# Kernel tuning notes

Hardware: AMD Instinct MI355X
Metric: run time of the kernel (lower is better)

## Reference

```python
import jax, jax.numpy as jnp
import numpy as np

B, H, W = 1, 1024, 2048
NX = 2048
H_STEP = 6.0 / NX            # h = length_x / nx
COF = 1.0                    # TEMPER_COEFFICIENT
DIFF = 0.0                   # self.diff_coeff
WC0V = 651.83 * 202.412 * 0.001 / 2.0   # wc0 = WC0*TH0*0.001/THcell
C1, C2, C4, N_EXP, CT = 0.65248278, 0.002, 400.0, 0.5, 1.0
FLUX0 = 300.0                # self.flux value used inside evp()

# 3x3 'valid' stencils on the reflect-padded field (match torch conv2d cross-correlation)
def _dx(x):
    return 0.5 * (x[..., 1:-1, 2:] - x[..., 1:-1, :-2])

def _dy(x):
    return 0.5 * (x[..., 2:, 1:-1] - x[..., :-2, 1:-1])

def _lap(x):
    return (x[..., 1:-1, 2:] + x[..., 1:-1, :-2] + x[..., 2:, 1:-1]
            + x[..., :-2, 1:-1] - 4.0 * x[..., 1:-1, 1:-1])

def _evp(tmp, wc_bc):
    t = tmp + 273.15
    cp_a = (28.11 + 1.967e-3 * t + 4.802e-6 * t**2 - 1.966e-9 * t**3) / 28.97 * 1000.0
    cp_v = (32.24 + 1.923e-3 * t + 10.55e-6 * t**2 - 3.595e-9 * t**3) / 18.015 * 1000.0
    P_v = jnp.exp(23.2 - 3816.4 / (t - 46.1))
    x_v = 0.62198 * P_v / (101325.0 - P_v)
    x_a = 0.00725
    C3 = jnp.power(jnp.mean(wc_bc) / WC0V, N_EXP)
    porous = C1 * C2 * C3 * C4 * CT
    m_dot = FLUX0 / (cp_a + cp_v * x_a) * (x_v - x_a) * porous
    return m_dot


def _forward(layout, heat_ini, wc, heat, flow):
    u = flow[..., 0, :, :]                      # [B,H,W]
    v = flow[..., 1, :, :]
    b = layout[:, 1].squeeze()                  # [H,W] int boundary codes
    geom = layout[:, 0].astype(heat.dtype)      # [B,H,W]
    geom = geom.at[..., 0, :].set(1.0).at[..., -1, :].set(1.0)
    # in-place boundary edits, same order as torch
    b = (b.at[1, 1:].set(0).at[-2, 1:].set(0).at[:, 1].set(0)
          .at[:, -1].set(3).at[0, :].set(3).at[-1, :].set(3))

    wc_mask = (b > 3).astype(wc.dtype)          # [H,W], broadcasts like torch [1,1,H,W]
    wc_bc = wc * wc_mask
    bc_mask = (b != 1).astype(heat.dtype)       # set_bc(1, tmp=0): mask 0, value 0
    heat_bc = heat * bc_mask

    xp = jnp.pad(heat_bc, ((0, 0), (0, 0), (1, 1), (1, 1)), mode='reflect')
    m_dot = _evp(heat_bc, wc_bc)                # evp called twice with identical state
    src = 300.0 * H_STEP                        # self.src (evp_src returns 0)
    flux = 300.0 * H_STEP                       # self.flux at apply_Energy time

    dx_, dy_ = _dx(xp), _dy(xp)                 # [B,1,H,W]
    ad = heat_ini - 0.001 * (u * dx_ + v * dy_ - DIFF * _lap(xp) / H_STEP)
    wcv = WC0V - 0.001 * m_dot                  # self.wc(wc)

    extras = {0: 0.0, 2: 0.0, 3: 0.0,
              4: flux * dx_ + wcv, 5: -flux * dy_ + wcv,
              6: -flux * dx_ + wcv, 7: flux * dy_ + wcv,
              8: flux * (-dx_ + dy_) + wcv, 9: flux * (dy_ + dx_) + wcv,
              10: flux * (dx_ - dy_) + wcv, 11: flux * (-dx_ - dy_) + wcv}
    loss_eq = jnp.zeros_like(heat)
    eq_mask = jnp.zeros_like(b)
    for eq in [0, 2, 3, 4, 5, 6, 7, 8, 9, 10, 11]:   # fixed small set, not a data dim
        m = (b == eq)
        eq_mask = jnp.where(m, eq, eq_mask)
        loss_eq = loss_eq + m.astype(heat.dtype) * (ad + extras[eq])

    f = COF * jnp.abs(geom - 1.0) * src * H_STEP     # [B,H,W]
    energy_loss = jnp.mean((loss_eq - f[:, None]) ** 2)
    wc_loss = jnp.mean((WC0V * wc_mask - m_dot - wc_bc) ** 2)
    return energy_loss + wc_loss, heat_bc, eq_mask


def setup_inputs() -> dict:
    key = jax.random.key(0)
    k1, k2, k3, k4, k5 = jax.random.split(key, 5)
    layout = jax.random.randint(k1, (B, 2, H, W), 0, 12, dtype=jnp.int32)
    heat_ini = jax.random.normal(k2, (B, 1, H, W), dtype=jnp.float32)
    wc = jax.random.uniform(k3, (B, 1, H, W), dtype=jnp.float32)
    heat = jax.random.normal(k4, (B, 1, H, W), dtype=jnp.float32)
    flow = jax.random.normal(k5, (B, 2, H, W), dtype=jnp.float32)
    return {"layout": layout, "heat_ini": heat_ini, "wc": wc, "heat": heat, "flow": flow}


def reference(layout, heat_ini, wc, heat, flow):
    return _forward(layout, heat_ini, wc, heat, flow)
```

## Files before the change

kernel.cpp:

```cpp
#include <hip/hip_runtime.h>
#include <math.h>

#define H_ 1024
#define W_ 2048
#define HW_ (H_ * W_)
#define NB_ 2048

#define FLUXF     0.87890625f
#define F_FACT    0.002574920654296875f
#define WC0VF     65.96910698f
#define POROUS_K  0.521986224f

__device__ __forceinline__ int fix_b(int raw, int i, int j) {
    if (i == 0 || i == H_ - 1) return 3;
    if (j == W_ - 1) return 3;
    if (j == 1) return 0;
    if ((i == 1 || i == H_ - 2) && j >= 1) return 0;
    return raw;
}

__global__ __launch_bounds__(256)
void k_main(const int* __restrict__ layout, const float* __restrict__ heat_ini,
            const float* __restrict__ wc, const float* __restrict__ heat,
            const float* __restrict__ flow, float* __restrict__ out_hb,
            float* __restrict__ out_eq, float* __restrict__ ws) {
    int gid  = blockIdx.x * 256 + threadIdx.x;
    int idx4 = gid << 2;
    int i  = idx4 >> 11;
    int jb = idx4 & (W_ - 1);
    int im = (i == 0) ? 1 : i - 1;
    int ip = (i == H_ - 1) ? H_ - 2 : i + 1;
    const int* L1 = layout + HW_;

    int4   bc4 = *(const int4*)(L1 + idx4);
    int4   bu4 = *(const int4*)(L1 + im * W_ + jb);
    int4   bd4 = *(const int4*)(L1 + ip * W_ + jb);
    int4   g4  = *(const int4*)(layout + idx4);
    float4 hc4 = *(const float4*)(heat + idx4);
    float4 hu4 = *(const float4*)(heat + im * W_ + jb);
    float4 hd4 = *(const float4*)(heat + ip * W_ + jb);
    float4 hi4 = *(const float4*)(heat_ini + idx4);
    float4 w4  = *(const float4*)(wc + idx4);
    float4 u4  = *(const float4*)(flow + idx4);
    float4 v4  = *(const float4*)(flow + HW_ + idx4);

    float hl = 0.0f, hr = 0.0f; int bl = 0, br = 0;
    if (jb != 0)      { hl = heat[idx4 - 1]; bl = L1[idx4 - 1]; }
    if (jb != W_ - 4) { hr = heat[idx4 + 4]; br = L1[idx4 + 4]; }

    int   bcs[4] = {bc4.x, bc4.y, bc4.z, bc4.w};
    int   bus[4] = {bu4.x, bu4.y, bu4.z, bu4.w};
    int   bds[4] = {bd4.x, bd4.y, bd4.z, bd4.w};
    int   gs[4]  = {g4.x, g4.y, g4.z, g4.w};
    float hcs[4] = {hc4.x, hc4.y, hc4.z, hc4.w};
    float hus[4] = {hu4.x, hu4.y, hu4.z, hu4.w};
    float hds[4] = {hd4.x, hd4.y, hd4.z, hd4.w};
    float his[4] = {hi4.x, hi4.y, hi4.z, hi4.w};
    float wss[4] = {w4.x, w4.y, w4.z, w4.w};
    float us[4]  = {u4.x, u4.y, u4.z, u4.w};
    float vs[4]  = {v4.x, v4.y, v4.z, v4.w};

    int bfix[4];
    float hb6[6];
    hb6[0] = (fix_b(bl, i, jb - 1) != 1) ? hl : 0.0f;
    hb6[5] = (fix_b(br, i, jb + 4) != 1) ? hr : 0.0f;
    float4 ohb, oeq;
    float* pohb = &ohb.x; float* poeq = &oeq.x;
    #pragma unroll
    for (int k = 0; k < 4; k++) {
        int b = fix_b(bcs[k], i, jb + k);
        bfix[k] = b;
        float hbv = (b != 1) ? hcs[k] : 0.0f;
        hb6[k + 1] = hbv;
        pohb[k] = hbv;
        poeq[k] = (b == 1) ? 0.0f : (float)b;
    }
    *(float4*)(out_hb + idx4) = ohb;
    *(float4*)(out_eq + idx4) = oeq;

    float acc[7] = {0.f, 0.f, 0.f, 0.f, 0.f, 0.f, 0.f};
    #pragma unroll
    for (int k = 0; k < 4; k++) {
        int j = jb + k;
        int b = bfix[k];
        float dx = 0.5f * (hb6[k + 2] - hb6[k]);
        if (j == 0 || j == W_ - 1) dx = 0.0f;
        float hbu = (fix_b(bus[k], im, j) != 1) ? hus[k] : 0.0f;
        float hbd = (fix_b(bds[k], ip, j) != 1) ? hds[k] : 0.0f;
        float dy = 0.5f * (hbd - hbu);

        float ad = his[k] - 0.001f * (us[k] * dx + vs[k] * dy);

        float t  = hb6[k + 1] + 273.15f;
        float t2 = t * t, t3 = t2 * t;
        float cp_a = (28.11f + 0.001967f * t + 4.802e-6f * t2 - 1.966e-9f * t3)
                     * (1000.0f / 28.97f);
        float cp_v = (32.24f + 0.001923f * t + 1.055e-5f * t2 - 3.595e-9f * t3)
                     * (1000.0f / 18.015f);
        float P_v = expf(23.2f - 3816.4f / (t - 46.1f));
        float x_v = 0.62198f * P_v / (101325.0f - P_v);
        float q = 300.0f / (cp_a + cp_v * 0.00725f) * (x_v - 0.00725f);

        float f = (i == 0 || i == H_ - 1) ? 0.0f
                  : fabsf((float)gs[k] - 1.0f) * F_FACT;

        float a_e, c_e;
        if (b == 1) {
            a_e = -f; c_e = 0.0f;
        } else {
            float cx = (b == 4 || b == 9 || b == 10) ? 1.0f
                     : ((b == 6 || b == 8 || b == 11) ? -1.0f : 0.0f);
            float cy = (b == 7 || b == 8 || b == 9) ? 1.0f
                     : ((b == 5 || b == 10 || b == 11) ? -1.0f : 0.0f);
            float extra0 = (b >= 4) ? (FLUXF * (cx * dx + cy * dy) + WC0VF) : 0.0f;
            a_e = ad + extra0 - f;
            c_e = (b >= 4) ? (-0.001f * q) : 0.0f;
        }
        acc[1] += a_e * a_e;
        acc[2] += a_e * c_e;
        acc[3] += c_e * c_e;

        float wm  = (b > 3) ? 1.0f : 0.0f;
        float wcb = wm * wss[k];
        float aw  = WC0VF * wm - wcb;
        acc[0] += wcb;
        acc[4] += aw * aw;
        acc[5] += aw * q;
        acc[6] += q * q;
    }

    #pragma unroll
    for (int off = 32; off > 0; off >>= 1) {
        #pragma unroll
        for (int s = 0; s < 7; s++) acc[s] += __shfl_down(acc[s], off, 64);
    }
    __shared__ float red[4][7];
    int lane = threadIdx.x & 63, wid = threadIdx.x >> 6;
    if (lane == 0) {
        #pragma unroll
        for (int s = 0; s < 7; s++) red[wid][s] = acc[s];
    }
    __syncthreads();
    if (threadIdx.x == 0) {
        #pragma unroll
        for (int s = 0; s < 7; s++)
            ws[s * NB_ + blockIdx.x] =
                red[0][s] + red[1][s] + red[2][s] + red[3][s];
    }
}

__global__ __launch_bounds__(256)
void k_final(const float* __restrict__ ws, float* __restrict__ out) {
    __shared__ float sred[7][4];
    int tid = threadIdx.x;
    #pragma unroll
    for (int s = 0; s < 7; s++) {
        float a = 0.0f;
        for (int t = tid; t < NB_; t += 256) a += ws[s * NB_ + t];
        #pragma unroll
        for (int off = 32; off > 0; off >>= 1) a += __shfl_down(a, off, 64);
        if ((tid & 63) == 0) sred[s][tid >> 6] = a;
    }
    __syncthreads();
    if (tid == 0) {
        float S[7];
        #pragma unroll
        for (int s = 0; s < 7; s++)
            S[s] = sred[s][0] + sred[s][1] + sred[s][2] + sred[s][3];
        float mean_wc = S[0] * (1.0f / (float)HW_);
        float p = POROUS_K * sqrtf(mean_wc / WC0VF);
        float energy = S[1] + 2.0f * p * S[2] + p * p * S[3];
        float wcl    = S[4] - 2.0f * p * S[5] + p * p * S[6];
        out[0] = (energy + wcl) * (1.0f / (float)HW_);
    }
}

extern "C" void kernel_launch(void* const* d_in, const int* in_sizes, int n_in,
                              void* d_out, int out_size, void* d_ws, size_t ws_size,
                              hipStream_t stream) {
    const int*   layout   = (const int*)d_in[0];
    const float* heat_ini = (const float*)d_in[1];
    const float* wc       = (const float*)d_in[2];
    const float* heat     = (const float*)d_in[3];
    const float* flow     = (const float*)d_in[4];
    float* out = (float*)d_out;
    float* ws  = (float*)d_ws;

    float* out_hb = out + 1;
    float* out_eq = out + 1 + HW_;

    k_main<<<NB_, 256, 0, stream>>>(layout, heat_ini, wc, heat, flow,
                                    out_hb, out_eq, ws);
    k_final<<<1, 256, 0, stream>>>(ws, out);
}
```

Measured before the change: 127.1 us.

## Map one block per row with 8 elements per thread and LDS halo exchange

Each block now covers one full image row and each thread handles 8 contiguous elements, using two float4 loads per array. The masked heat row is staged in shared memory so the left and right neighbours for the x-derivative come from LDS rather than scalar global loads. The block count is halved, and the final reduction reads one float4 per thread. This adds a __syncthreads and raises register pressure from the doubled per-thread state.

```diff
diff --git a/kernel.cpp b/kernel.cpp
--- a/kernel.cpp
+++ b/kernel.cpp
@@ -4,7 +4,7 @@
 #define H_ 1024
 #define W_ 2048
 #define HW_ (H_ * W_)
-#define NB_ 2048
+#define NB_ 1024
 
 #define FLUXF     0.87890625f
 #define F_FACT    0.002574920654296875f
@@ -24,74 +24,72 @@
             const float* __restrict__ wc, const float* __restrict__ heat,
             const float* __restrict__ flow, float* __restrict__ out_hb,
             float* __restrict__ out_eq, float* __restrict__ ws) {
-    int gid  = blockIdx.x * 256 + threadIdx.x;
-    int idx4 = gid << 2;
-    int i  = idx4 >> 11;
-    int jb = idx4 & (W_ - 1);
-    int im = (i == 0) ? 1 : i - 1;
-    int ip = (i == H_ - 1) ? H_ - 2 : i + 1;
+    const int i  = blockIdx.x;
+    const int jb = threadIdx.x << 3;
+    const int im = (i == 0) ? 1 : i - 1;
+    const int ip = (i == H_ - 1) ? H_ - 2 : i + 1;
     const int* L1 = layout + HW_;
+    const int base  = i * W_ + jb;
+    const int baseu = im * W_ + jb;
+    const int based = ip * W_ + jb;
 
-    int4   bc4 = *(const int4*)(L1 + idx4);
-    int4   bu4 = *(const int4*)(L1 + im * W_ + jb);
-    int4   bd4 = *(const int4*)(L1 + ip * W_ + jb);
-    int4   g4  = *(const int4*)(layout + idx4);
-    float4 hc4 = *(const float4*)(heat + idx4);
-    float4 hu4 = *(const float4*)(heat + im * W_ + jb);
-    float4 hd4 = *(const float4*)(heat + ip * W_ + jb);
-    float4 hi4 = *(const float4*)(heat_ini + idx4);
-    float4 w4  = *(const float4*)(wc + idx4);
-    float4 u4  = *(const float4*)(flow + idx4);
-    float4 v4  = *(const float4*)(flow + HW_ + idx4);
+    int4   bc0 = *(const int4*)(L1 + base),      bc1 = *(const int4*)(L1 + base + 4);
+    int4   bu0 = *(const int4*)(L1 + baseu),     bu1 = *(const int4*)(L1 + baseu + 4);
+    int4   bd0 = *(const int4*)(L1 + based),     bd1 = *(const int4*)(L1 + based + 4);
+    int4   g0  = *(const int4*)(layout + base),  g1  = *(const int4*)(layout + base + 4);
+    float4 hc0 = *(const float4*)(heat + base),  hc1 = *(const float4*)(heat + base + 4);
+    float4 hu0 = *(const float4*)(heat + baseu), hu1 = *(const float4*)(heat + baseu + 4);
+    float4 hd0 = *(const float4*)(heat + based), hd1 = *(const float4*)(heat + based + 4);
+    float4 hi0 = *(const float4*)(heat_ini + base), hi1 = *(const float4*)(heat_ini + base + 4);
+    float4 w0  = *(const float4*)(wc + base),    w1  = *(const float4*)(wc + base + 4);
+    float4 u0  = *(const float4*)(flow + base),  u1  = *(const float4*)(flow + base + 4);
+    float4 v0  = *(const float4*)(flow + HW_ + base), v1 = *(const float4*)(flow + HW_ + base + 4);
 
-    float hl = 0.0f, hr = 0.0f; int bl = 0, br = 0;
-    if (jb != 0)      { hl = heat[idx4 - 1]; bl = L1[idx4 - 1]; }
-    if (jb != W_ - 4) { hr = heat[idx4 + 4]; br = L1[idx4 + 4]; }
+    int   bcs[8] = {bc0.x,bc0.y,bc0.z,bc0.w, bc1.x,bc1.y,bc1.z,bc1.w};
+    int   bus[8] = {bu0.x,bu0.y,bu0.z,bu0.w, bu1.x,bu1.y,bu1.z,bu1.w};
+    int   bds[8] = {bd0.x,bd0.y,bd0.z,bd0.w, bd1.x,bd1.y,bd1.z,bd1.w};
+    int   gs[8]  = {g0.x,g0.y,g0.z,g0.w, g1.x,g1.y,g1.z,g1.w};
+    float hcs[8] = {hc0.x,hc0.y,hc0.z,hc0.w, hc1.x,hc1.y,hc1.z,hc1.w};
+    float hus[8] = {hu0.x,hu0.y,hu0.z,hu0.w, hu1.x,hu1.y,hu1.z,hu1.w};
+    float hds[8] = {hd0.x,hd0.y,hd0.z,hd0.w, hd1.x,hd1.y,hd1.z,hd1.w};
+    float his[8] = {hi0.x,hi0.y,hi0.z,hi0.w, hi1.x,hi1.y,hi1.z,hi1.w};
+    float wss[8] = {w0.x,w0.y,w0.z,w0.w, w1.x,w1.y,w1.z,w1.w};
+    float us[8]  = {u0.x,u0.y,u0.z,u0.w, u1.x,u1.y,u1.z,u1.w};
+    float vs[8]  = {v0.x,v0.y,v0.z,v0.w, v1.x,v1.y,v1.z,v1.w};
 
-    int   bcs[4] = {bc4.x, bc4.y, bc4.z, bc4.w};
-    int   bus[4] = {bu4.x, bu4.y, bu4.z, bu4.w};
-    int   bds[4] = {bd4.x, bd4.y, bd4.z, bd4.w};
-    int   gs[4]  = {g4.x, g4.y, g4.z, g4.w};
-    float hcs[4] = {hc4.x, hc4.y, hc4.z, hc4.w};
-    float hus[4] = {hu4.x, hu4.y, hu4.z, hu4.w};
-    float hds[4] = {hd4.x, hd4.y, hd4.z, hd4.w};
-    float his[4] = {hi4.x, hi4.y, hi4.z, hi4.w};
-    float wss[4] = {w4.x, w4.y, w4.z, w4.w};
-    float us[4]  = {u4.x, u4.y, u4.z, u4.w};
-    float vs[4]  = {v4.x, v4.y, v4.z, v4.w};
-
-    int bfix[4];
-    float hb6[6];
-    hb6[0] = (fix_b(bl, i, jb - 1) != 1) ? hl : 0.0f;
-    hb6[5] = (fix_b(br, i, jb + 4) != 1) ? hr : 0.0f;
-    float4 ohb, oeq;
-    float* pohb = &ohb.x; float* poeq = &oeq.x;
+    __shared__ float shb[W_];
+    int   bfix[8];
+    float hb8[8], oeqs[8];
     #pragma unroll
-    for (int k = 0; k < 4; k++) {
+    for (int k = 0; k < 8; k++) {
         int b = fix_b(bcs[k], i, jb + k);
         bfix[k] = b;
-        float hbv = (b != 1) ? hcs[k] : 0.0f;
-        hb6[k + 1] = hbv;
-        pohb[k] = hbv;
-        poeq[k] = (b == 1) ? 0.0f : (float)b;
+        hb8[k]  = (b != 1) ? hcs[k] : 0.0f;
+        oeqs[k] = (b == 1) ? 0.0f : (float)b;
     }
-    *(float4*)(out_hb + idx4) = ohb;
-    *(float4*)(out_eq + idx4) = oeq;
+    *(float4*)(shb + jb)     = make_float4(hb8[0], hb8[1], hb8[2], hb8[3]);
+    *(float4*)(shb + jb + 4) = make_float4(hb8[4], hb8[5], hb8[6], hb8[7]);
+    *(float4*)(out_hb + base)     = make_float4(hb8[0], hb8[1], hb8[2], hb8[3]);
+    *(float4*)(out_hb + base + 4) = make_float4(hb8[4], hb8[5], hb8[6], hb8[7]);
+    *(float4*)(out_eq + base)     = make_float4(oeqs[0], oeqs[1], oeqs[2], oeqs[3]);
+    *(float4*)(out_eq + base + 4) = make_float4(oeqs[4], oeqs[5], oeqs[6], oeqs[7]);
+    __syncthreads();
 
-    float acc[7] = {0.f, 0.f, 0.f, 0.f, 0.f, 0.f, 0.f};
+    float acc[7] = {0.f,0.f,0.f,0.f,0.f,0.f,0.f};
     #pragma unroll
-    for (int k = 0; k < 4; k++) {
+    for (int k = 0; k < 8; k++) {
         int j = jb + k;
         int b = bfix[k];
-        float dx = 0.5f * (hb6[k + 2] - hb6[k]);
-        if (j == 0 || j == W_ - 1) dx = 0.0f;
+        float hl = (k == 0) ? ((j == 0) ? 0.0f : shb[j - 1]) : hb8[k - 1];
+        float hr = (k == 7) ? ((j == W_ - 1) ? 0.0f : shb[j + 1]) : hb8[k + 1];
+        float dx = (j == 0 || j == W_ - 1) ? 0.0f : 0.5f * (hr - hl);
         float hbu = (fix_b(bus[k], im, j) != 1) ? hus[k] : 0.0f;
         float hbd = (fix_b(bds[k], ip, j) != 1) ? hds[k] : 0.0f;
         float dy = 0.5f * (hbd - hbu);
 
         float ad = his[k] - 0.001f * (us[k] * dx + vs[k] * dy);
 
-        float t  = hb6[k + 1] + 273.15f;
+        float t  = hb8[k] + 273.15f;
         float t2 = t * t, t3 = t2 * t;
         float cp_a = (28.11f + 0.001967f * t + 4.802e-6f * t2 - 1.966e-9f * t3)
                      * (1000.0f / 28.97f);
@@ -155,8 +153,8 @@
     int tid = threadIdx.x;
     #pragma unroll
     for (int s = 0; s < 7; s++) {
-        float a = 0.0f;
-        for (int t = tid; t < NB_; t += 256) a += ws[s * NB_ + t];
+        float4 x = *(const float4*)(ws + s * NB_ + (tid << 2));
+        float a = x.x + x.y + x.z + x.w;
         #pragma unroll
         for (int off = 32; off > 0; off >>= 1) a += __shfl_down(a, off, 64);
         if ((tid & 63) == 0) sred[s][tid >> 6] = a;
```

After: 114.7 us. 1.11x faster.
